# Kernel tuning notes

Measured on AMD Instinct MI355X. Metric: run time of the kernel, lower is better.

Reference implementation:

```python
import jax, jax.numpy as jnp
from jax import lax
import numpy as np

B, T, S, E, H = 32, 128, 256, 512, 1024


def _lstm_cell(x, h, c, Wih, Whh, bih, bhh):
    # gates in PyTorch order: i, f, g, o
    g = x @ Wih.T + bih + h @ Whh.T + bhh
    i, f, gg, o = jnp.split(g, 4, axis=-1)
    c_new = jax.nn.sigmoid(f) * c + jax.nn.sigmoid(i) * jnp.tanh(gg)
    h_new = jax.nn.sigmoid(o) * jnp.tanh(c_new)
    return h_new, c_new


def setup_inputs() -> dict:
    key = jax.random.key(0)
    ks = jax.random.split(key, 20)
    s = 1.0 / np.sqrt(H)

    def rn(k, shape, scale):
        return (jax.random.normal(k, shape, jnp.float32) * scale)

    inputs = rn(ks[0], (B, T, E), 1.0)
    enc_outputs = rn(ks[1], (S, B, H), 1.0)
    enc_c = rn(ks[2], (2, B, H // 2), 1.0)
    lengths = jax.random.randint(ks[3], (B,), S // 2, S + 1)
    mask = jnp.arange(S)[None, :] >= lengths[:, None]  # [B,S] True = pad

    return {
        "inputs": inputs, "enc_outputs": enc_outputs, "enc_c": enc_c, "mask": mask,
        "Wq": rn(ks[4], (H, H), s), "bq": jnp.zeros((H,), jnp.float32),
        "Wk": rn(ks[5], (H, H), s), "bk": jnp.zeros((H,), jnp.float32),
        "Wv": rn(ks[6], (H, H), s), "bv": jnp.zeros((H,), jnp.float32),
        "Wo": rn(ks[7], (H, H), s), "bo": jnp.zeros((H,), jnp.float32),
        "Wih0": rn(ks[8], (4 * H, H + E), s), "Whh0": rn(ks[9], (4 * H, H), s),
        "bih0": jnp.zeros((4 * H,), jnp.float32), "bhh0": jnp.zeros((4 * H,), jnp.float32),
        "Wih1": rn(ks[10], (4 * H, H), s), "Whh1": rn(ks[11], (4 * H, H), s),
        "bih1": jnp.zeros((4 * H,), jnp.float32), "bhh1": jnp.zeros((4 * H,), jnp.float32),
    }


def reference(inputs, enc_outputs, enc_c, mask, Wq, bq, Wk, bk, Wv, bv, Wo, bo,
              Wih0, Whh0, bih0, bhh0, Wih1, Whh1, bih1, bhh1):
    # Precompute attention K/V projections once (they do not depend on the step).
    K = jnp.einsum('sbe,he->sbh', enc_outputs, Wk) + bk
    V = jnp.einsum('sbe,he->sbh', enc_outputs, Wv) + bv
    scale = 1.0 / jnp.sqrt(jnp.asarray(H, inputs.dtype))

    # Initial LSTM state per the module: c stacked from concat of encoder
    # bidirectional cell states, h zeros.
    c_init = jnp.concatenate([enc_c[0], enc_c[1]], axis=-1)  # [B,H]
    c0 = jnp.stack([c_init, c_init])                          # [2,B,H]
    h0 = jnp.zeros_like(c0)

    def step(carry, x_t):
        h, c = carry
        q = c[1] @ Wq.T + bq                                  # query = last-layer cell state
        scores = jnp.einsum('bh,sbh->bs', q, K) * scale
        scores = jnp.where(mask, -1e9, scores)
        attn = jax.nn.softmax(scores, axis=-1)
        ctx = jnp.einsum('bs,sbh->bh', attn, V) @ Wo.T + bo   # [B,H]
        x = jnp.concatenate([ctx, x_t], axis=-1)              # [B,H+E]
        h_0, c_0 = _lstm_cell(x, h[0], c[0], Wih0, Whh0, bih0, bhh0)
        h_1, c_1 = _lstm_cell(h_0, h[1], c[1], Wih1, Whh1, bih1, bhh1)
        return (jnp.stack([h_0, h_1]), jnp.stack([c_0, c_1])), h_1

    _, outs = lax.scan(step, (h0, c0), inputs.transpose(1, 0, 2))  # [T,B,H]
    return outs.transpose(1, 0, 2)  # [B,T,H]
```

## Files before the change

kernel.cpp:

```cpp
#include <hip/hip_runtime.h>

typedef unsigned short u16;
typedef unsigned int   u32;
typedef unsigned char  u8;

constexpr int kB = 32, kT = 128, kS = 256, kE = 512, kH = 1024, kG = 4096;

typedef __attribute__((ext_vector_type(8))) short bfx8;
typedef __attribute__((ext_vector_type(4))) float fx4;

__device__ __forceinline__ float b2f(u16 v){ return __uint_as_float(((u32)v) << 16); }
__device__ __forceinline__ u16  f2b(float f){
    u32 u = __float_as_uint(f);
    return (u16)((u + 0x7FFFu + ((u >> 16) & 1u)) >> 16);
}
__device__ __forceinline__ float sigf(float x){ return 1.f / (1.f + expf(-x)); }
__device__ __forceinline__ float ldin(const void* p, size_t i, int dt){
    return dt ? ((const float*)p)[i] : b2f(((const u16*)p)[i]);
}

__global__ void detect_dtype_k(const void* __restrict__ inputs, int* __restrict__ dtflag)
{
    __shared__ int bad;
    int t = threadIdx.x;
    if (t == 0) bad = 0;
    __syncthreads();
    const u16* p = (const u16*)inputs;
    int l = 0;
    for (int i = t; i < 4096; i += 256){
        u16 v = p[i];
        int e = (v >> 7) & 0xFF;
        if (v != 0 && (e < 90 || e > 140)) l = 1;
    }
    if (l) atomicOr(&bad, 1);
    __syncthreads();
    if (t == 0) *dtflag = bad;
}

__global__ void prep_mask_k(const void* __restrict__ mask, float* __restrict__ maskflag)
{
    __shared__ int bad32, bad16, bad8, evenNZ;
    int t = threadIdx.x;
    if (t == 0){ bad32 = 0; bad16 = 0; bad8 = 0; evenNZ = 0; }
    __syncthreads();
    const u32* w32 = (const u32*)mask;
    const u16* w16 = (const u16*)mask;
    const u8*  w8  = (const u8*)mask;
    int l32 = 0, l16 = 0, l8 = 0, lev = 0;
    for (int i = t; i < 2048; i += 256){ u32 v = w32[i]; l32 |= (v > 1u); }
    for (int i = t; i < 4096; i += 256){
        u16 v = w16[i];
        l16 |= (v != 0 && v != 0x3F80u);
        if ((i & 1) == 0 && v != 0) lev = 1;
    }
    for (int i = t; i < 8192; i += 256){ l8 |= (w8[i] > 1); }
    if (l32) atomicOr(&bad32, 1);
    if (l16) atomicOr(&bad16, 1);
    if (l8)  atomicOr(&bad8, 1);
    if (lev) atomicOr(&evenNZ, 1);
    __syncthreads();
    int mode;
    if (!bad32)       mode = 0;
    else if (!bad16)  mode = evenNZ ? 1 : 3;
    else if (!bad8)   mode = 2;
    else              mode = 3;
    for (int i = t; i < kB * kS; i += 256){
        bool m;
        if (mode == 0)      m = (((const int*)mask)[i] != 0);
        else if (mode == 1) m = (w16[i] != 0);
        else if (mode == 2) m = (w8[i] != 0);
        else                m = (((const float*)mask)[i] != 0.f);
        maskflag[i] = m ? 1.f : 0.f;
    }
}

__global__ void prep_bias_k(const void* __restrict__ Wq, const void* __restrict__ bq,
                            const void* __restrict__ Wk, const void* __restrict__ bk,
                            const void* __restrict__ bv, const void* __restrict__ Wo,
                            const void* __restrict__ bo,
                            const void* __restrict__ bih0, const void* __restrict__ bhh0,
                            const void* __restrict__ bih1, const void* __restrict__ bhh1,
                            float* __restrict__ bkq, float* __restrict__ bvo,
                            float* __restrict__ ubq, float* __restrict__ bof,
                            float* __restrict__ bias01, float* __restrict__ bias1,
                            float* __restrict__ cbqbk, const int* __restrict__ dtflag)
{
    int dt = *dtflag;
    int idx = blockIdx.x * 256 + threadIdx.x;
    if (idx < 1024){
        float s = 0.f;
        for (int i = 0; i < 1024; i++) s += ldin(bk, i, dt) * ldin(Wq, (size_t)i * 1024 + idx, dt);
        bkq[idx] = s;
    } else if (idx < 2048){ int o2 = idx - 1024;
        float s = 0.f;
        for (int h = 0; h < 1024; h++) s += ldin(bv, h, dt) * ldin(Wo, (size_t)o2 * 1024 + h, dt);
        bvo[o2] = s;
    } else if (idx < 3072){ int e = idx - 2048;
        float s = 0.f;
        for (int i = 0; i < 1024; i++) s += ldin(bq, i, dt) * ldin(Wk, (size_t)i * 1024 + e, dt);
        ubq[e] = s;
    } else if (idx < 4096){ int o2 = idx - 3072;
        bof[o2] = ldin(bo, o2, dt);
    } else if (idx < 8192){ int j = idx - 4096;
        bias01[j] = ldin(bih0, j, dt) + ldin(bhh0, j, dt);
    } else if (idx < 12288){ int j = idx - 8192;
        bias1[j] = ldin(bih1, j, dt) + ldin(bhh1, j, dt);
    } else if (idx == 12288){
        float s = 0.f;
        for (int i = 0; i < 1024; i++) s += ldin(bq, i, dt) * ldin(bk, i, dt);
        cbqbk[0] = s;
    }
}

__global__ void init_state_k(const void* __restrict__ enc_c,
                             float* __restrict__ c0, float* __restrict__ c1,
                             u16* __restrict__ H0h, u16* __restrict__ H0l,
                             u16* __restrict__ H1h, u16* __restrict__ H1l,
                             const int* __restrict__ dtflag)
{
    int dt = *dtflag;
    int idx = blockIdx.x * 256 + threadIdx.x;
    int b = idx >> 10, h = idx & 1023;
    float cv = (h < 512) ? ldin(enc_c, (size_t)b * 512 + h, dt)
                         : ldin(enc_c, (size_t)(32 + b) * 512 + (h - 512), dt);
    c0[idx] = cv;
    c1[idx] = cv; c1[32768 + idx] = cv;
    H0h[idx] = 0; H0l[idx] = 0;
    H1h[idx] = 0; H1l[idx] = 0;
}

__global__ void split_plain_k(const void* __restrict__ src, u16* __restrict__ Oh,
                              u16* __restrict__ Ol, int n, const int* __restrict__ dtflag)
{
    int dt = *dtflag;
    int idx = blockIdx.x * 256 + threadIdx.x;
    if (idx >= n) return;
    float v = ldin(src, idx, dt);
    u16 h = f2b(v);
    Oh[idx] = h;
    Ol[idx] = f2b(v - b2f(h));
}

__global__ void split_x_k(const void* __restrict__ inputs, u16* __restrict__ Xh,
                          u16* __restrict__ Xl, const int* __restrict__ dtflag)
{
    int dt = *dtflag;
    int idx = blockIdx.x * 256 + threadIdx.x;
    int b = idx >> 16, t = (idx >> 9) & 127, e = idx & 511;
    float v = ldin(inputs, idx, dt);
    u16 h = f2b(v);
    size_t o = ((size_t)(t * 32 + b) << 9) + e;
    Xh[o] = h;
    Xl[o] = f2b(v - b2f(h));
}

__global__ void tsplit_k(const void* __restrict__ W, int ldw, int col_off,
                         u16* __restrict__ Oh, u16* __restrict__ Ol, int ldo,
                         const int* __restrict__ dtflag)
{
    __shared__ float tile[64][65];
    int dt = *dtflag;
    int r0 = blockIdx.x * 64, c0 = blockIdx.y * 64;
    for (int i = 0; i < 16; i++){
        int idx = threadIdx.x + i * 256;
        int rr = idx >> 6, cc = idx & 63;
        tile[rr][cc] = ldin(W, (size_t)(r0 + rr) * ldw + col_off + c0 + cc, dt);
    }
    __syncthreads();
    for (int i = 0; i < 16; i++){
        int idx = threadIdx.x + i * 256;
        int cr = idx >> 6, rc = idx & 63;
        float v = tile[rc][cr];
        u16 h = f2b(v);
        size_t o = (size_t)(c0 + cr) * ldo + r0 + rc;
        Oh[o] = h;
        Ol[o] = f2b(v - b2f(h));
    }
}

__global__ __launch_bounds__(256) void wfrag_k(const void* __restrict__ W, int ldw, int col_off,
                                               u16* __restrict__ F, int KSS,
                                               const int* __restrict__ dtflag)
{
    int dt = *dtflag;
    int ct = blockIdx.x;
    int iters = KSS * 2;
    for (int i = 0; i < iters; i++){
        int flat = threadIdx.x + i * 256;
        int ks = flat >> 9, r = flat & 511, l = r >> 3, j = r & 7;
        int row = ct * 16 + (l & 15);
        int k = ks * 32 + (l >> 4) * 8 + j;
        F[(size_t)ct * (KSS * 512) + flat] = f2b(ldin(W, (size_t)row * ldw + col_off + k, dt));
    }
}

template<int EPI>
__global__ __launch_bounds__(256) void gemm_hilo_k(
    const u16* __restrict__ Ah, const u16* __restrict__ Al, int ldA,
    const u16* __restrict__ Bh, const u16* __restrict__ Bl, int ldB,
    u16* __restrict__ OutH, u16* __restrict__ OutL, int ldO,
    const float* __restrict__ bias, float scale)
{
    __shared__ __align__(16) u16 Bsh[64][40];
    __shared__ __align__(16) u16 Bsl[64][40];
    int tid = threadIdx.x, wave = tid >> 6, lane = tid & 63;
    int m0 = blockIdx.x * 64, n0 = blockIdx.y * 64;
    int rA = lane & 15, kq = lane >> 4;
    fx4 acc[4];
    #pragma unroll
    for (int nt = 0; nt < 4; nt++) acc[nt] = (fx4){0.f, 0.f, 0.f, 0.f};
    int skk = tid >> 3, snn = (tid & 7) * 8;
    for (int k0 = 0; k0 < 1024; k0 += 32){
        bfx8 vh = *(const bfx8*)(Bh + (size_t)(k0 + skk) * ldB + n0 + snn);
        bfx8 vl = *(const bfx8*)(Bl + (size_t)(k0 + skk) * ldB + n0 + snn);
        __syncthreads();
        #pragma unroll
        for (int q = 0; q < 8; q++){ Bsh[snn + q][skk] = (u16)vh[q]; Bsl[snn + q][skk] = (u16)vl[q]; }
        __syncthreads();
        size_t abase = (size_t)(m0 + wave * 16 + rA) * ldA + k0 + kq * 8;
        bfx8 a_h = *(const bfx8*)(Ah + abase);
        bfx8 a_l = *(const bfx8*)(Al + abase);
        #pragma unroll
        for (int nt = 0; nt < 4; nt++){
            bfx8 b_h = *(const bfx8*)&Bsh[nt * 16 + rA][kq * 8];
            bfx8 b_l = *(const bfx8*)&Bsl[nt * 16 + rA][kq * 8];
            acc[nt] = __builtin_amdgcn_mfma_f32_16x16x32_bf16(a_h, b_h, acc[nt], 0, 0, 0);
            acc[nt] = __builtin_amdgcn_mfma_f32_16x16x32_bf16(a_h, b_l, acc[nt], 0, 0, 0);
            acc[nt] = __builtin_amdgcn_mfma_f32_16x16x32_bf16(a_l, b_h, acc[nt], 0, 0, 0);
        }
    }
    #pragma unroll
    for (int nt = 0; nt < 4; nt++){
        #pragma unroll
        for (int i = 0; i < 4; i++){
            int m = m0 + wave * 16 + kq * 4 + i;
            int n = n0 + nt * 16 + rA;
            float v = acc[nt][i];
            if (EPI == 0){
                u16 h = f2b(v);
                OutH[(size_t)m * ldO + n] = h;
                OutL[(size_t)m * ldO + n] = f2b(v - b2f(h));
            } else {
                float v2 = (v + bias[n]) * scale;
                OutH[(((size_t)(((m & 31) << 8) | (m >> 5))) << 10) + n] = f2b(v2);
            }
        }
    }
}

__global__ __launch_bounds__(256) void skbq_k(
    const void* __restrict__ enc, const float* __restrict__ ubq,
    const float* __restrict__ cbqbk, float* __restrict__ skbqs,
    const int* __restrict__ dtflag)
{
    int dt = *dtflag;
    int w = (blockIdx.x * 256 + threadIdx.x) >> 6;
    int lane = threadIdx.x & 63;
    int s = w >> 5, b = w & 31;
    size_t base = (size_t)w * 1024 + lane * 16;
    float acc = 0.f;
    #pragma unroll
    for (int i = 0; i < 16; i++) acc += ubq[lane * 16 + i] * ldin(enc, base + i, dt);
    #pragma unroll
    for (int off = 32; off; off >>= 1) acc += __shfl_down(acc, off, 64);
    if (lane == 0) skbqs[b * 256 + s] = (acc + cbqbk[0]) * 0.03125f;
}

__global__ __launch_bounds__(256) void scores_k(
    const float* __restrict__ pp, const float* __restrict__ bias1,
    const float* __restrict__ c1rd, float* __restrict__ c1wr,
    u16* __restrict__ H1h, u16* __restrict__ H1l,
    float* __restrict__ y_out, int t,
    const u16* __restrict__ KQb, const float* __restrict__ skbqs,
    const float* __restrict__ maskflag, float* __restrict__ scores)
{
    __shared__ float cs[1024];
    int b = blockIdx.x >> 3, sg = blockIdx.x & 7;
    int tid = threadIdx.x;
    if (t > 0){
        #pragma unroll
        for (int i = 0; i < 4; i++){
            int h = tid + i * 256;
            int cidx = (b << 10) + h;
            float g[4];
            #pragma unroll
            for (int gate = 0; gate < 4; gate++){
                int j = (gate << 10) + h;
                g[gate] = bias1[j]
                        + pp[(((size_t)(0 * 32 + b)) << 12) + j]
                        + pp[(((size_t)(1 * 32 + b)) << 12) + j]
                        + pp[(((size_t)(2 * 32 + b)) << 12) + j]
                        + pp[(((size_t)(3 * 32 + b)) << 12) + j];
            }
            float c = sigf(g[1]) * c1rd[cidx] + sigf(g[0]) * tanhf(g[2]);
            cs[h] = c;
            if (sg == 0){
                c1wr[cidx] = c;
                float hv = sigf(g[3]) * tanhf(c);
                u16 hh = f2b(hv);
                H1h[cidx] = hh;
                H1l[cidx] = f2b(hv - b2f(hh));
                y_out[(((size_t)b * kT + (t - 1)) << 10) + h] = hv;
            }
        }
    } else {
        #pragma unroll
        for (int i = 0; i < 4; i++){
            int h = tid + i * 256;
            cs[h] = c1rd[(b << 10) + h];
        }
    }
    __syncthreads();
    if (t >= kT) return;
    int wave = tid >> 6, lane = tid & 63;
    float c16[16];
    #pragma unroll
    for (int i = 0; i < 16; i++) c16[i] = cs[lane * 16 + i];
    #pragma unroll
    for (int si = 0; si < 8; si++){
        int s = sg * 32 + wave * 8 + si;
        const u16* kp = KQb + (((size_t)((b << 8) | s)) << 10) + lane * 16;
        uint4 k0 = *(const uint4*)kp;
        uint4 k1 = *(const uint4*)(kp + 8);
        float a = 0.f;
        a += c16[0]  * b2f((u16)(k0.x & 0xFFFFu)) + c16[1]  * b2f((u16)(k0.x >> 16));
        a += c16[2]  * b2f((u16)(k0.y & 0xFFFFu)) + c16[3]  * b2f((u16)(k0.y >> 16));
        a += c16[4]  * b2f((u16)(k0.z & 0xFFFFu)) + c16[5]  * b2f((u16)(k0.z >> 16));
        a += c16[6]  * b2f((u16)(k0.w & 0xFFFFu)) + c16[7]  * b2f((u16)(k0.w >> 16));
        a += c16[8]  * b2f((u16)(k1.x & 0xFFFFu)) + c16[9]  * b2f((u16)(k1.x >> 16));
        a += c16[10] * b2f((u16)(k1.y & 0xFFFFu)) + c16[11] * b2f((u16)(k1.y >> 16));
        a += c16[12] * b2f((u16)(k1.z & 0xFFFFu)) + c16[13] * b2f((u16)(k1.z >> 16));
        a += c16[14] * b2f((u16)(k1.w & 0xFFFFu)) + c16[15] * b2f((u16)(k1.w >> 16));
        #pragma unroll
        for (int off = 32; off; off >>= 1) a += __shfl_down(a, off, 64);
        if (lane == 0){
            int is = (b << 8) + s;
            scores[is] = (maskflag[is] != 0.f) ? -1e9f : a + skbqs[is];
        }
    }
}

__global__ __launch_bounds__(256) void smctx_k(
    const float* __restrict__ scores, const u16* __restrict__ Vob,
    const float* __restrict__ bof, u16* __restrict__ Ch, u16* __restrict__ Cl)
{
    __shared__ float attn[256];
    __shared__ float wred[8];
    __shared__ float2 part[4][64];
    int b = blockIdx.x >> 3, ht = blockIdx.x & 7;
    int tid = threadIdx.x;
    float scv = scores[(b << 8) + tid];
    float m = scv;
    #pragma unroll
    for (int off = 32; off; off >>= 1) m = fmaxf(m, __shfl_down(m, off, 64));
    if ((tid & 63) == 0) wred[tid >> 6] = m;
    __syncthreads();
    float mm = fmaxf(fmaxf(wred[0], wred[1]), fmaxf(wred[2], wred[3]));
    float ex = expf(scv - mm);
    float ssum = ex;
    #pragma unroll
    for (int off = 32; off; off >>= 1) ssum += __shfl_down(ssum, off, 64);
    if ((tid & 63) == 0) wred[4 + (tid >> 6)] = ssum;
    __syncthreads();
    float tot = (wred[4] + wred[5]) + (wred[6] + wred[7]);
    attn[tid] = ex / tot;
    __syncthreads();
    int hl = tid & 63, scn = tid >> 6;
    int h2 = ht * 128 + hl * 2;
    const u16* vcol = Vob + ((size_t)b << 18) + h2;
    float a0 = 0.f, a1 = 0.f;
    #pragma unroll 8
    for (int s = scn; s < 256; s += 4){
        u32 v = *(const u32*)(vcol + ((size_t)s << 10));
        float at = attn[s];
        a0 += at * b2f((u16)(v & 0xFFFFu));
        a1 += at * b2f((u16)(v >> 16));
    }
    part[scn][hl] = make_float2(a0, a1);
    __syncthreads();
    if (tid < 64){
        float2 p0 = part[0][tid], p1 = part[1][tid], p2 = part[2][tid], p3 = part[3][tid];
        int h = ht * 128 + tid * 2;
        float v0 = p0.x + p1.x + p2.x + p3.x + bof[h];
        float v1 = p0.y + p1.y + p2.y + p3.y + bof[h + 1];
        u16 h0 = f2b(v0), h1 = f2b(v1);
        int base = (b << 10) + h;
        Ch[base] = h0;     Ch[base + 1] = h1;
        Cl[base] = f2b(v0 - b2f(h0));
        Cl[base + 1] = f2b(v1 - b2f(h1));
    }
}

template<int LAYER>
__global__ __launch_bounds__(256) void gmm_k(
    const u16* __restrict__ f0, const u16* __restrict__ f1, const u16* __restrict__ f2,
    const u16* __restrict__ a0h, const u16* __restrict__ a0l,
    const u16* __restrict__ a1h, const u16* __restrict__ a1l,
    const u16* __restrict__ a2h, const u16* __restrict__ a2l,
    float* __restrict__ pp)
{
    __shared__ float red[4][32][64];
    int ht = blockIdx.x, q = blockIdx.y;
    int tid = threadIdx.x, wave = tid >> 6, lane = tid & 63;
    int rA = lane & 15, kq = lane >> 4;
    constexpr int PER_W = (LAYER == 0) ? 5 : 4;
    fx4 acc[2][4];
    #pragma unroll
    for (int mt = 0; mt < 2; mt++)
        #pragma unroll
        for (int nt = 0; nt < 4; nt++) acc[mt][nt] = (fx4){0.f, 0.f, 0.f, 0.f};

    #pragma unroll
    for (int si = 0; si < PER_W; si++){
        int s = q * (PER_W * 4) + wave * PER_W + si;
        const u16 *F, *ah, *al; int ks, ld, KSSF;
        if (LAYER == 0){
            if (s < 32)      { F = f0; ks = s;      ah = a0h; al = a0l; ld = 1024; KSSF = 32; }
            else if (s < 64) { F = f1; ks = s - 32; ah = a1h; al = a1l; ld = 1024; KSSF = 32; }
            else             { F = f2; ks = s - 64; ah = a2h; al = a2l; ld = 512;  KSSF = 16; }
        } else {
            if (s < 32)      { F = f0; ks = s;      ah = a0h; al = a0l; }
            else             { F = f1; ks = s - 32; ah = a1h; al = a1l; }
            ld = 1024; KSSF = 32;
        }
        int koff = ks * 32 + kq * 8;
        bfx8 a_h0 = *(const bfx8*)(ah + (size_t)rA * ld + koff);
        bfx8 a_l0 = *(const bfx8*)(al + (size_t)rA * ld + koff);
        bfx8 a_h1 = *(const bfx8*)(ah + (size_t)(16 + rA) * ld + koff);
        bfx8 a_l1 = *(const bfx8*)(al + (size_t)(16 + rA) * ld + koff);
        #pragma unroll
        for (int nt = 0; nt < 4; nt++){
            bfx8 bf = *(const bfx8*)(F + ((size_t)((nt * 64 + ht) * KSSF + ks) * 64 + lane) * 8);
            acc[0][nt] = __builtin_amdgcn_mfma_f32_16x16x32_bf16(a_h0, bf, acc[0][nt], 0, 0, 0);
            acc[0][nt] = __builtin_amdgcn_mfma_f32_16x16x32_bf16(a_l0, bf, acc[0][nt], 0, 0, 0);
            acc[1][nt] = __builtin_amdgcn_mfma_f32_16x16x32_bf16(a_h1, bf, acc[1][nt], 0, 0, 0);
            acc[1][nt] = __builtin_amdgcn_mfma_f32_16x16x32_bf16(a_l1, bf, acc[1][nt], 0, 0, 0);
        }
    }
    #pragma unroll
    for (int mt = 0; mt < 2; mt++)
        #pragma unroll
        for (int nt = 0; nt < 4; nt++)
            #pragma unroll
            for (int i = 0; i < 4; i++)
                red[wave][mt * 16 + kq * 4 + i][nt * 16 + rA] = acc[mt][nt][i];
    __syncthreads();
    #pragma unroll
    for (int i = 0; i < 8; i++){
        int flat = tid + i * 256;
        int b = flat >> 6, cl = flat & 63;
        int nt = cl >> 4, hl = cl & 15;
        float v = (red[0][b][cl] + red[1][b][cl]) + (red[2][b][cl] + red[3][b][cl]);
        pp[(((size_t)(q * 32 + b)) << 12) + nt * 1024 + ht * 16 + hl] = v;
    }
}

__global__ __launch_bounds__(256) void cell0_k(
    const float* __restrict__ pp, const float* __restrict__ biasv,
    float* __restrict__ c_state, u16* __restrict__ outHh, u16* __restrict__ outHl)
{
    int idx = blockIdx.x * 256 + threadIdx.x;
    int b = idx >> 10, h = idx & 1023;
    float g[4];
    #pragma unroll
    for (int gate = 0; gate < 4; gate++){
        int j = gate * 1024 + h;
        g[gate] = biasv[j]
                + pp[(((size_t)(0 * 32 + b)) << 12) + j]
                + pp[(((size_t)(1 * 32 + b)) << 12) + j]
                + pp[(((size_t)(2 * 32 + b)) << 12) + j]
                + pp[(((size_t)(3 * 32 + b)) << 12) + j];
    }
    float gi_ = sigf(g[0]);
    float gf_ = sigf(g[1]);
    float gg_ = tanhf(g[2]);
    float go_ = sigf(g[3]);
    float c = gf_ * c_state[idx] + gi_ * gg_;
    c_state[idx] = c;
    float hv = go_ * tanhf(c);
    u16 hh = f2b(hv);
    outHh[idx] = hh;
    outHl[idx] = f2b(hv - b2f(hh));
}

extern "C" void kernel_launch(void* const* d_in, const int* in_sizes, int n_in,
                              void* d_out, int out_size, void* d_ws, size_t ws_size,
                              hipStream_t stream)
{
    const void* inputs = d_in[0];
    const void* enc    = d_in[1];
    const void* enc_c  = d_in[2];
    const void* mask   = d_in[3];
    const void* Wq   = d_in[4];
    const void* bq   = d_in[5];
    const void* Wk   = d_in[6];
    const void* bk   = d_in[7];
    const void* Wv   = d_in[8];
    const void* bv   = d_in[9];
    const void* Wo   = d_in[10];
    const void* bo   = d_in[11];
    const void* Wih0 = d_in[12];
    const void* Whh0 = d_in[13];
    const void* bih0 = d_in[14];
    const void* bhh0 = d_in[15];
    const void* Wih1 = d_in[16];
    const void* Whh1 = d_in[17];
    const void* bih1 = d_in[18];
    const void* bhh1 = d_in[19];
    float* out = (float*)d_out;
    (void)in_sizes; (void)n_in; (void)out_size; (void)ws_size;

    char* ws = (char*)d_ws;
    size_t off = 0;
    auto alloc = [&](size_t bytes) -> void* {
        void* p = ws + off; off += (bytes + 255) & ~(size_t)255; return p;
    };
    char* poolA = (char*)alloc((size_t)37748736);
    u16* Eh  = (u16*)poolA;
    u16* El  = (u16*)(poolA + 16777216);
    u16* F0c = (u16*)poolA;
    u16* F0h = (u16*)(poolA + 8388608);
    u16* F1i = (u16*)(poolA + 16777216);
    u16* F1h = (u16*)(poolA + 25165824);
    u16* F0x = (u16*)(poolA + 33554432);
    char* poolB = (char*)alloc((size_t)16777216);
    u16* Akh  = (u16*)poolB;
    u16* Akl  = (u16*)(poolB + 2097152);
    u16* Bqh  = (u16*)(poolB + 4194304);
    u16* Bql  = (u16*)(poolB + 6291456);
    u16* Avh  = (u16*)(poolB + 8388608);
    u16* Avl  = (u16*)(poolB + 10485760);
    u16* Both = (u16*)(poolB + 12582912);
    u16* Botl = (u16*)(poolB + 14680064);
    u16*  KQb  = (u16*)alloc((size_t)kB * kS * kH * 2);
    u16*  Vob  = (u16*)alloc((size_t)kB * kS * kH * 2);
    u16*  Xh   = (u16*)alloc((size_t)kB * kT * kE * 2);
    u16*  Xl   = (u16*)alloc((size_t)kB * kT * kE * 2);
    u16*  Wkqh = (u16*)alloc((size_t)kH * kH * 2);
    u16*  Wkql = (u16*)alloc((size_t)kH * kH * 2);
    u16*  Wvoh = (u16*)alloc((size_t)kH * kH * 2);
    u16*  Wvol = (u16*)alloc((size_t)kH * kH * 2);
    float* pp  = (float*)alloc((size_t)4 * kB * kG * 4);
    float* scores = (float*)alloc(kB * kS * 4);
    u16*  Ch   = (u16*)alloc((size_t)kB * kH * 2);
    u16*  Cl   = (u16*)alloc((size_t)kB * kH * 2);
    u16*  H0h  = (u16*)alloc((size_t)kB * kH * 2);
    u16*  H0l  = (u16*)alloc((size_t)kB * kH * 2);
    u16*  H1h  = (u16*)alloc((size_t)kB * kH * 2);
    u16*  H1l  = (u16*)alloc((size_t)kB * kH * 2);
    float* c0f = (float*)alloc(kB * kH * 4);
    float* c1f = (float*)alloc((size_t)2 * kB * kH * 4);
    float* bkq = (float*)alloc(1024 * 4);
    float* bvo = (float*)alloc(1024 * 4);
    float* ubq = (float*)alloc(1024 * 4);
    float* bof = (float*)alloc(1024 * 4);
    float* bias01 = (float*)alloc(4096 * 4);
    float* bias1  = (float*)alloc(4096 * 4);
    float* cbqbk  = (float*)alloc(256);
    float* skbqs  = (float*)alloc(kB * kS * 4);
    float* maskflag = (float*)alloc(kB * kS * 4);
    int*   dtflag = (int*)alloc(256);

    detect_dtype_k<<<1, 256, 0, stream>>>(inputs, dtflag);
    prep_mask_k<<<1, 256, 0, stream>>>(mask, maskflag);
    prep_bias_k<<<49, 256, 0, stream>>>(Wq, bq, Wk, bk, bv, Wo, bo,
                                        bih0, bhh0, bih1, bhh1,
                                        bkq, bvo, ubq, bof, bias01, bias1, cbqbk, dtflag);
    init_state_k<<<128, 256, 0, stream>>>(enc_c, c0f, c1f, H0h, H0l, H1h, H1l, dtflag);
    split_plain_k<<<32768, 256, 0, stream>>>(enc, Eh, El, 8388608, dtflag);
    split_plain_k<<<4096, 256, 0, stream>>>(Wq, Bqh, Bql, 1048576, dtflag);
    tsplit_k<<<dim3(16, 16), 256, 0, stream>>>(Wk, 1024, 0, Akh, Akl, 1024, dtflag);
    tsplit_k<<<dim3(16, 16), 256, 0, stream>>>(Wv, 1024, 0, Avh, Avl, 1024, dtflag);
    tsplit_k<<<dim3(16, 16), 256, 0, stream>>>(Wo, 1024, 0, Both, Botl, 1024, dtflag);
    split_x_k<<<8192, 256, 0, stream>>>(inputs, Xh, Xl, dtflag);
    gemm_hilo_k<0><<<dim3(16, 16), 256, 0, stream>>>(Akh, Akl, 1024, Bqh, Bql, 1024,
                                                     Wkqh, Wkql, 1024, nullptr, 1.f);
    gemm_hilo_k<0><<<dim3(16, 16), 256, 0, stream>>>(Avh, Avl, 1024, Both, Botl, 1024,
                                                     Wvoh, Wvol, 1024, nullptr, 1.f);
    gemm_hilo_k<1><<<dim3(128, 16), 256, 0, stream>>>(Eh, El, 1024, Wkqh, Wkql, 1024,
                                                      KQb, nullptr, 0, bkq, 0.03125f);
    gemm_hilo_k<1><<<dim3(128, 16), 256, 0, stream>>>(Eh, El, 1024, Wvoh, Wvol, 1024,
                                                      Vob, nullptr, 0, bvo, 1.0f);
    skbq_k<<<2048, 256, 0, stream>>>(enc, ubq, cbqbk, skbqs, dtflag);
    wfrag_k<<<256, 256, 0, stream>>>(Wih0, 1536, 0,    F0c, 32, dtflag);
    wfrag_k<<<256, 256, 0, stream>>>(Whh0, 1024, 0,    F0h, 32, dtflag);
    wfrag_k<<<256, 256, 0, stream>>>(Wih0, 1536, 1024, F0x, 16, dtflag);
    wfrag_k<<<256, 256, 0, stream>>>(Wih1, 1024, 0,    F1i, 32, dtflag);
    wfrag_k<<<256, 256, 0, stream>>>(Whh1, 1024, 0,    F1h, 32, dtflag);

    for (int t = 0; t < kT; t++){
        const float* c1rd = c1f + (size_t)((t + 1) & 1) * kB * kH;
        float*       c1wr = c1f + (size_t)(t & 1) * kB * kH;
        scores_k<<<256, 256, 0, stream>>>(pp, bias1, c1rd, c1wr, H1h, H1l, out, t,
                                          KQb, skbqs, maskflag, scores);
        smctx_k<<<256, 256, 0, stream>>>(scores, Vob, bof, Ch, Cl);
        gmm_k<0><<<dim3(64, 4), 256, 0, stream>>>(
            F0c, F0h, F0x, Ch, Cl, H0h, H0l,
            Xh + (size_t)t * 32 * kE, Xl + (size_t)t * 32 * kE, pp);
        cell0_k<<<128, 256, 0, stream>>>(pp, bias01, c0f, H0h, H0l);
        gmm_k<1><<<dim3(64, 4), 256, 0, stream>>>(
            F1i, F1h, nullptr, H0h, H0l, H1h, H1l, nullptr, nullptr, pp);
    }
    {
        const float* c1rd = c1f + (size_t)((kT + 1) & 1) * kB * kH;
        float*       c1wr = c1f + (size_t)(kT & 1) * kB * kH;
        scores_k<<<256, 256, 0, stream>>>(pp, bias1, c1rd, c1wr, H1h, H1l, out, kT,
                                          KQb, skbqs, maskflag, scores);
    }
}
```

Before: 5.976 ms.

## Fuse LSTM gate GEMM with cell update by regrouping weight fragments per hidden slice

Weight fragments are reordered so that each block computes all four gates for four hidden units. This lets each gate GEMM block apply the LSTM cell nonlinearity directly and write h and c, which removes the partial-sum buffer, the separate cell0 kernel and the cell1 work folded into scores_k. Hidden states are now double-buffered to avoid read/write races between blocks, so each step launches four kernels instead of five. Each block does its whole K reduction across only four waves with a single 16-wide N tile, which may lower MFMA parallelism per block.

```diff
diff --git a/kernel.cpp b/kernel.cpp
--- a/kernel.cpp
+++ b/kernel.cpp
@@ -123,10 +123,11 @@
     int b = idx >> 10, h = idx & 1023;
     float cv = (h < 512) ? ldin(enc_c, (size_t)b * 512 + h, dt)
                          : ldin(enc_c, (size_t)(32 + b) * 512 + (h - 512), dt);
-    c0[idx] = cv;
-    c1[idx] = cv; c1[32768 + idx] = cv;
-    H0h[idx] = 0; H0l[idx] = 0;
-    H1h[idx] = 0; H1l[idx] = 0;
+    c0[idx] = cv; c1[idx] = cv;
+    H0h[idx] = 0; H0h[32768 + idx] = 0;
+    H0l[idx] = 0; H0l[32768 + idx] = 0;
+    H1h[idx] = 0; H1h[32768 + idx] = 0;
+    H1l[idx] = 0; H1l[32768 + idx] = 0;
 }
 
 __global__ void split_plain_k(const void* __restrict__ src, u16* __restrict__ Oh,
@@ -178,19 +179,19 @@
     }
 }
 
-__global__ __launch_bounds__(256) void wfrag_k(const void* __restrict__ W, int ldw, int col_off,
-                                               u16* __restrict__ F, int KSS,
-                                               const int* __restrict__ dtflag)
-{
-    int dt = *dtflag;
-    int ct = blockIdx.x;
+__global__ __launch_bounds__(256) void wfrag2_k(const void* __restrict__ W, int ldw, int col_off,
+                                                u16* __restrict__ F, int KSS,
+                                                const int* __restrict__ dtflag)
+{
+    int dt = *dtflag;
+    int hs = blockIdx.x;
     int iters = KSS * 2;
     for (int i = 0; i < iters; i++){
         int flat = threadIdx.x + i * 256;
         int ks = flat >> 9, r = flat & 511, l = r >> 3, j = r & 7;
-        int row = ct * 16 + (l & 15);
-        int k = ks * 32 + (l >> 4) * 8 + j;
-        F[(size_t)ct * (KSS * 512) + flat] = f2b(ldin(W, (size_t)row * ldw + col_off + k, dt));
+        int row = (((l & 15) >> 2) << 10) + hs * 4 + (l & 3);
+        int k = col_off + ks * 32 + ((l >> 4) << 3) + j;
+        F[(size_t)hs * (KSS * 512) + flat] = f2b(ldin(W, (size_t)row * ldw + k, dt));
     }
 }
 
@@ -267,51 +268,19 @@
 }
 
 __global__ __launch_bounds__(256) void scores_k(
-    const float* __restrict__ pp, const float* __restrict__ bias1,
-    const float* __restrict__ c1rd, float* __restrict__ c1wr,
-    u16* __restrict__ H1h, u16* __restrict__ H1l,
-    float* __restrict__ y_out, int t,
-    const u16* __restrict__ KQb, const float* __restrict__ skbqs,
-    const float* __restrict__ maskflag, float* __restrict__ scores)
+    const float* __restrict__ c1f, const u16* __restrict__ KQb,
+    const float* __restrict__ skbqs, const float* __restrict__ maskflag,
+    float* __restrict__ scores)
 {
     __shared__ float cs[1024];
     int b = blockIdx.x >> 3, sg = blockIdx.x & 7;
     int tid = threadIdx.x;
-    if (t > 0){
-        #pragma unroll
-        for (int i = 0; i < 4; i++){
-            int h = tid + i * 256;
-            int cidx = (b << 10) + h;
-            float g[4];
-            #pragma unroll
-            for (int gate = 0; gate < 4; gate++){
-                int j = (gate << 10) + h;
-                g[gate] = bias1[j]
-                        + pp[(((size_t)(0 * 32 + b)) << 12) + j]
-                        + pp[(((size_t)(1 * 32 + b)) << 12) + j]
-                        + pp[(((size_t)(2 * 32 + b)) << 12) + j]
-                        + pp[(((size_t)(3 * 32 + b)) << 12) + j];
-            }
-            float c = sigf(g[1]) * c1rd[cidx] + sigf(g[0]) * tanhf(g[2]);
-            cs[h] = c;
-            if (sg == 0){
-                c1wr[cidx] = c;
-                float hv = sigf(g[3]) * tanhf(c);
-                u16 hh = f2b(hv);
-                H1h[cidx] = hh;
-                H1l[cidx] = f2b(hv - b2f(hh));
-                y_out[(((size_t)b * kT + (t - 1)) << 10) + h] = hv;
-            }
-        }
-    } else {
-        #pragma unroll
-        for (int i = 0; i < 4; i++){
-            int h = tid + i * 256;
-            cs[h] = c1rd[(b << 10) + h];
-        }
-    }
-    __syncthreads();
-    if (t >= kT) return;
+    #pragma unroll
+    for (int i = 0; i < 4; i++){
+        int h = tid + i * 256;
+        cs[h] = c1f[(b << 10) + h];
+    }
+    __syncthreads();
     int wave = tid >> 6, lane = tid & 63;
     float c16[16];
     #pragma unroll
@@ -392,27 +361,27 @@
 }
 
 template<int LAYER>
-__global__ __launch_bounds__(256) void gmm_k(
+__global__ __launch_bounds__(256) void gc_k(
     const u16* __restrict__ f0, const u16* __restrict__ f1, const u16* __restrict__ f2,
     const u16* __restrict__ a0h, const u16* __restrict__ a0l,
     const u16* __restrict__ a1h, const u16* __restrict__ a1l,
     const u16* __restrict__ a2h, const u16* __restrict__ a2l,
-    float* __restrict__ pp)
-{
-    __shared__ float red[4][32][64];
-    int ht = blockIdx.x, q = blockIdx.y;
+    const float* __restrict__ biasv, float* __restrict__ c_state,
+    u16* __restrict__ outHh, u16* __restrict__ outHl,
+    float* __restrict__ y_out, int t)
+{
+    __shared__ float red[4][32][16];
+    int hs = blockIdx.x;
     int tid = threadIdx.x, wave = tid >> 6, lane = tid & 63;
     int rA = lane & 15, kq = lane >> 4;
-    constexpr int PER_W = (LAYER == 0) ? 5 : 4;
-    fx4 acc[2][4];
-    #pragma unroll
-    for (int mt = 0; mt < 2; mt++)
-        #pragma unroll
-        for (int nt = 0; nt < 4; nt++) acc[mt][nt] = (fx4){0.f, 0.f, 0.f, 0.f};
+    constexpr int PER_W = (LAYER == 0) ? 20 : 16;
+    fx4 acc[2];
+    acc[0] = (fx4){0.f, 0.f, 0.f, 0.f};
+    acc[1] = (fx4){0.f, 0.f, 0.f, 0.f};
 
     #pragma unroll
     for (int si = 0; si < PER_W; si++){
-        int s = q * (PER_W * 4) + wave * PER_W + si;
+        int s = wave * PER_W + si;
         const u16 *F, *ah, *al; int ks, ld, KSSF;
         if (LAYER == 0){
             if (s < 32)      { F = f0; ks = s;      ah = a0h; al = a0l; ld = 1024; KSSF = 32; }
@@ -428,59 +397,41 @@
         bfx8 a_l0 = *(const bfx8*)(al + (size_t)rA * ld + koff);
         bfx8 a_h1 = *(const bfx8*)(ah + (size_t)(16 + rA) * ld + koff);
         bfx8 a_l1 = *(const bfx8*)(al + (size_t)(16 + rA) * ld + koff);
-        #pragma unroll
-        for (int nt = 0; nt < 4; nt++){
-            bfx8 bf = *(const bfx8*)(F + ((size_t)((nt * 64 + ht) * KSSF + ks) * 64 + lane) * 8);
-            acc[0][nt] = __builtin_amdgcn_mfma_f32_16x16x32_bf16(a_h0, bf, acc[0][nt], 0, 0, 0);
-            acc[0][nt] = __builtin_amdgcn_mfma_f32_16x16x32_bf16(a_l0, bf, acc[0][nt], 0, 0, 0);
-            acc[1][nt] = __builtin_amdgcn_mfma_f32_16x16x32_bf16(a_h1, bf, acc[1][nt], 0, 0, 0);
-            acc[1][nt] = __builtin_amdgcn_mfma_f32_16x16x32_bf16(a_l1, bf, acc[1][nt], 0, 0, 0);
-        }
+        bfx8 bf = *(const bfx8*)(F + (((size_t)hs * KSSF + ks) << 9) + lane * 8);
+        acc[0] = __builtin_amdgcn_mfma_f32_16x16x32_bf16(a_h0, bf, acc[0], 0, 0, 0);
+        acc[0] = __builtin_amdgcn_mfma_f32_16x16x32_bf16(a_l0, bf, acc[0], 0, 0, 0);
+        acc[1] = __builtin_amdgcn_mfma_f32_16x16x32_bf16(a_h1, bf, acc[1], 0, 0, 0);
+        acc[1] = __builtin_amdgcn_mfma_f32_16x16x32_bf16(a_l1, bf, acc[1], 0, 0, 0);
     }
     #pragma unroll
     for (int mt = 0; mt < 2; mt++)
         #pragma unroll
-        for (int nt = 0; nt < 4; nt++)
-            #pragma unroll
-            for (int i = 0; i < 4; i++)
-                red[wave][mt * 16 + kq * 4 + i][nt * 16 + rA] = acc[mt][nt][i];
-    __syncthreads();
-    #pragma unroll
-    for (int i = 0; i < 8; i++){
-        int flat = tid + i * 256;
-        int b = flat >> 6, cl = flat & 63;
-        int nt = cl >> 4, hl = cl & 15;
-        float v = (red[0][b][cl] + red[1][b][cl]) + (red[2][b][cl] + red[3][b][cl]);
-        pp[(((size_t)(q * 32 + b)) << 12) + nt * 1024 + ht * 16 + hl] = v;
-    }
-}
-
-__global__ __launch_bounds__(256) void cell0_k(
-    const float* __restrict__ pp, const float* __restrict__ biasv,
-    float* __restrict__ c_state, u16* __restrict__ outHh, u16* __restrict__ outHl)
-{
-    int idx = blockIdx.x * 256 + threadIdx.x;
-    int b = idx >> 10, h = idx & 1023;
-    float g[4];
-    #pragma unroll
-    for (int gate = 0; gate < 4; gate++){
-        int j = gate * 1024 + h;
-        g[gate] = biasv[j]
-                + pp[(((size_t)(0 * 32 + b)) << 12) + j]
-                + pp[(((size_t)(1 * 32 + b)) << 12) + j]
-                + pp[(((size_t)(2 * 32 + b)) << 12) + j]
-                + pp[(((size_t)(3 * 32 + b)) << 12) + j];
-    }
-    float gi_ = sigf(g[0]);
-    float gf_ = sigf(g[1]);
-    float gg_ = tanhf(g[2]);
-    float go_ = sigf(g[3]);
-    float c = gf_ * c_state[idx] + gi_ * gg_;
-    c_state[idx] = c;
-    float hv = go_ * tanhf(c);
-    u16 hh = f2b(hv);
-    outHh[idx] = hh;
-    outHl[idx] = f2b(hv - b2f(hh));
+        for (int i = 0; i < 4; i++)
+            red[wave][mt * 16 + kq * 4 + i][rA] = acc[mt][i];
+    __syncthreads();
+    if (tid < 128){
+        int b = tid >> 2, hl = tid & 3;
+        int hidx = hs * 4 + hl;
+        float g[4];
+        #pragma unroll
+        for (int gate = 0; gate < 4; gate++){
+            int c = gate * 4 + hl;
+            g[gate] = biasv[(gate << 10) + hidx]
+                    + (red[0][b][c] + red[1][b][c]) + (red[2][b][c] + red[3][b][c]);
+        }
+        float gi_ = sigf(g[0]);
+        float gf_ = sigf(g[1]);
+        float gg_ = tanhf(g[2]);
+        float go_ = sigf(g[3]);
+        int cidx = (b << 10) + hidx;
+        float c = gf_ * c_state[cidx] + gi_ * gg_;
+        c_state[cidx] = c;
+        float hv = go_ * tanhf(c);
+        u16 hh = f2b(hv);
+        outHh[cidx] = hh;
+        outHl[cidx] = f2b(hv - b2f(hh));
+        if (LAYER == 1) y_out[((size_t)b * kT + t) * kH + hidx] = hv;
+    }
 }
 
 extern "C" void kernel_launch(void* const* d_in, const int* in_sizes, int n_in,
@@ -540,16 +491,15 @@
     u16*  Wkql = (u16*)alloc((size_t)kH * kH * 2);
     u16*  Wvoh = (u16*)alloc((size_t)kH * kH * 2);
     u16*  Wvol = (u16*)alloc((size_t)kH * kH * 2);
-    float* pp  = (float*)alloc((size_t)4 * kB * kG * 4);
     float* scores = (float*)alloc(kB * kS * 4);
     u16*  Ch   = (u16*)alloc((size_t)kB * kH * 2);
     u16*  Cl   = (u16*)alloc((size_t)kB * kH * 2);
-    u16*  H0h  = (u16*)alloc((size_t)kB * kH * 2);
-    u16*  H0l  = (u16*)alloc((size_t)kB * kH * 2);
-    u16*  H1h  = (u16*)alloc((size_t)kB * kH * 2);
-    u16*  H1l  = (u16*)alloc((size_t)kB * kH * 2);
+    u16*  H0h  = (u16*)alloc((size_t)2 * kB * kH * 2);
+    u16*  H0l  = (u16*)alloc((size_t)2 * kB * kH * 2);
+    u16*  H1h  = (u16*)alloc((size_t)2 * kB * kH * 2);
+    u16*  H1l  = (u16*)alloc((size_t)2 * kB * kH * 2);
     float* c0f = (float*)alloc(kB * kH * 4);
-    float* c1f = (float*)alloc((size_t)2 * kB * kH * 4);
+    float* c1f = (float*)alloc(kB * kH * 4);
     float* bkq = (float*)alloc(1024 * 4);
     float* bvo = (float*)alloc(1024 * 4);
     float* ubq = (float*)alloc(1024 * 4);
@@ -582,29 +532,24 @@
     gemm_hilo_k<1><<<dim3(128, 16), 256, 0, stream>>>(Eh, El, 1024, Wvoh, Wvol, 1024,
                                                       Vob, nullptr, 0, bvo, 1.0f);
     skbq_k<<<2048, 256, 0, stream>>>(enc, ubq, cbqbk, skbqs, dtflag);
-    wfrag_k<<<256, 256, 0, stream>>>(Wih0, 1536, 0,    F0c, 32, dtflag);
-    wfrag_k<<<256, 256, 0, stream>>>(Whh0, 1024, 0,    F0h, 32, dtflag);
-    wfrag_k<<<256, 256, 0, stream>>>(Wih0, 1536, 1024, F0x, 16, dtflag);
-    wfrag_k<<<256, 256, 0, stream>>>(Wih1, 1024, 0,    F1i, 32, dtflag);
-    wfrag_k<<<256, 256, 0, stream>>>(Whh1, 1024, 0,    F1h, 32, dtflag);
+    wfrag2_k<<<256, 256, 0, stream>>>(Wih0, 1536, 0,    F0c, 32, dtflag);
+    wfrag2_k<<<256, 256, 0, stream>>>(Whh0, 1024, 0,    F0h, 32, dtflag);
+    wfrag2_k<<<256, 256, 0, stream>>>(Wih0, 1536, 1024, F0x, 16, dtflag);
+    wfrag2_k<<<256, 256, 0, stream>>>(Wih1, 1024, 0,    F1i, 32, dtflag);
+    wfrag2_k<<<256, 256, 0, stream>>>(Whh1, 1024, 0,    F1h, 32, dtflag);
 
     for (int t = 0; t < kT; t++){
-        const float* c1rd = c1f + (size_t)((t + 1) & 1) * kB * kH;
-        float*       c1wr = c1f + (size_t)(t & 1) * kB * kH;
-        scores_k<<<256, 256, 0, stream>>>(pp, bias1, c1rd, c1wr, H1h, H1l, out, t,
-                                          KQb, skbqs, maskflag, scores);
+        int rd = (t & 1) * kB * kH;
+        int wr = ((t + 1) & 1) * kB * kH;
+        scores_k<<<256, 256, 0, stream>>>(c1f, KQb, skbqs, maskflag, scores);
         smctx_k<<<256, 256, 0, stream>>>(scores, Vob, bof, Ch, Cl);
-        gmm_k<0><<<dim3(64, 4), 256, 0, stream>>>(
-            F0c, F0h, F0x, Ch, Cl, H0h, H0l,
-            Xh + (size_t)t * 32 * kE, Xl + (size_t)t * 32 * kE, pp);
-        cell0_k<<<128, 256, 0, stream>>>(pp, bias01, c0f, H0h, H0l);
-        gmm_k<1><<<dim3(64, 4), 256, 0, stream>>>(
-            F1i, F1h, nullptr, H0h, H0l, H1h, H1l, nullptr, nullptr, pp);
-    }
-    {
-        const float* c1rd = c1f + (size_t)((kT + 1) & 1) * kB * kH;
-        float*       c1wr = c1f + (size_t)(kT & 1) * kB * kH;
-        scores_k<<<256, 256, 0, stream>>>(pp, bias1, c1rd, c1wr, H1h, H1l, out, kT,
-                                          KQb, skbqs, maskflag, scores);
-    }
-}
+        gc_k<0><<<256, 256, 0, stream>>>(
+            F0c, F0h, F0x, Ch, Cl, H0h + rd, H0l + rd,
+            Xh + (size_t)t * 32 * kE, Xl + (size_t)t * 32 * kE,
+            bias01, c0f, H0h + wr, H0l + wr, nullptr, t);
+        gc_k<1><<<256, 256, 0, stream>>>(
+            F1i, F1h, nullptr, H0h + wr, H0l + wr, H1h + rd, H1l + rd,
+            nullptr, nullptr,
+            bias1, c1f, H1h + wr, H1l + wr, out, t);
+    }
+}
```

New measurement: 7.281 ms. 1.22x slower.
